# Optimization experiments

Measured on AMD Instinct MI355X. Metric: run time of the kernel, lower is better.

Reference implementation:

```python
import jax, jax.numpy as jnp
import numpy as np

B, C, H, W = 16, 64, 128, 128

def setup_inputs() -> dict:
    key = jax.random.key(0)
    k1, k2, k3 = jax.random.split(key, 3)
    pre = jax.random.normal(k1, (B, C, H, W), dtype=jnp.float32)
    gt = jax.random.normal(k2, (B, C, H, W), dtype=jnp.float32)
    mask = jax.random.randint(k3, (B, C, H, W), 0, 2).astype(jnp.float32)
    return {"pre": pre, "gt": gt, "mask": mask, "batch_size": B}

def reference(pre, gt, mask, batch_size):
    # per-(batch, channel) masked L1 sum, normalized by nonzero count of mask
    # (count clamped to >= 1), summed over all (b, c), divided by batch_size.
    masked_l1 = jnp.sum(jnp.abs(pre - gt) * mask, axis=(2, 3))          # [B, C]
    nonzero = jnp.sum((mask != 0).astype(pre.dtype), axis=(2, 3))       # [B, C]
    denom = jnp.maximum(nonzero, 1.0)
    loss = jnp.sum(masked_l1 / denom) / batch_size
    return loss
```

## Files before the change

### kernel.cpp

```cpp
#include <hip/hip_runtime.h>


#define HW_ELEMS 16384
#define HW_VEC4  4096
#define NBC      1024

__global__ __launch_bounds__(256) void l1_partial_kernel(
    const float* __restrict__ pre,
    const float* __restrict__ gt,
    const float* __restrict__ mask,
    float* __restrict__ ws) {
    const int bc = blockIdx.x;
    const size_t base = (size_t)bc * HW_ELEMS;
    const float4* __restrict__ p4 = (const float4*)(pre + base);
    const float4* __restrict__ g4 = (const float4*)(gt  + base);
    const float4* __restrict__ m4 = (const float4*)(mask + base);

    float s   = 0.0f;
    float cnt = 0.0f;

    for (int i = threadIdx.x; i < HW_VEC4; i += 256) {
        const float4 p = p4[i];
        const float4 g = g4[i];
        const float4 m = m4[i];
        s += fabsf(p.x - g.x) * m.x
           + fabsf(p.y - g.y) * m.y
           + fabsf(p.z - g.z) * m.z
           + fabsf(p.w - g.w) * m.w;
        cnt += (float)(m.x != 0.0f) + (float)(m.y != 0.0f)
             + (float)(m.z != 0.0f) + (float)(m.w != 0.0f);
    }

    #pragma unroll
    for (int off = 32; off > 0; off >>= 1) {
        s   += __shfl_down(s,   off, 64);
        cnt += __shfl_down(cnt, off, 64);
    }

    __shared__ float ss[4];
    __shared__ float sc[4];
    const int wave = threadIdx.x >> 6;
    const int lane = threadIdx.x & 63;
    if (lane == 0) { ss[wave] = s; sc[wave] = cnt; }
    __syncthreads();
    if (threadIdx.x == 0) {
        const float S  = ss[0] + ss[1] + ss[2] + ss[3];
        const float Cn = sc[0] + sc[1] + sc[2] + sc[3];
        ws[bc] = S / fmaxf(Cn, 1.0f);
    }
}

__global__ __launch_bounds__(256) void l1_final_kernel(
    const float* __restrict__ ws,
    const int* __restrict__ bsz,
    float* __restrict__ out) {
    float s = 0.0f;
    for (int i = threadIdx.x; i < NBC; i += 256) s += ws[i];
    #pragma unroll
    for (int off = 32; off > 0; off >>= 1) s += __shfl_down(s, off, 64);
    __shared__ float ss[4];
    const int wave = threadIdx.x >> 6;
    const int lane = threadIdx.x & 63;
    if (lane == 0) ss[wave] = s;
    __syncthreads();
    if (threadIdx.x == 0) {
        out[0] = (ss[0] + ss[1] + ss[2] + ss[3]) / (float)bsz[0];
    }
}

extern "C" void kernel_launch(void* const* d_in, const int* in_sizes, int n_in,
                              void* d_out, int out_size, void* d_ws, size_t ws_size,
                              hipStream_t stream) {
    const float* pre  = (const float*)d_in[0];
    const float* gt   = (const float*)d_in[1];
    const float* mask = (const float*)d_in[2];
    const int*   bsz  = (const int*)d_in[3];
    float* ws  = (float*)d_ws;
    float* out = (float*)d_out;

    l1_partial_kernel<<<NBC, 256, 0, stream>>>(pre, gt, mask, ws);
    l1_final_kernel<<<1, 256, 0, stream>>>(ws, bsz, out);
}
```

Baseline: 200.8 us.

## Split each (b,c) plane across four blocks and batch loads per thread

Each (batch, channel) plane is now handled by four blocks instead of one, giving 4096 blocks to fill the GPU. Each block writes a partial sum and a partial mask count, and the final kernel combines them before normalising. Every thread issues all twelve float4 loads up front to raise memory-level parallelism. The cost is more workspace traffic and a slightly heavier final reduction.

```diff
diff --git a/kernel.cpp b/kernel.cpp
--- a/kernel.cpp
+++ b/kernel.cpp
@@ -1,34 +1,42 @@
 #include <hip/hip_runtime.h>
 
 
-#define HW_ELEMS 16384
-#define HW_VEC4  4096
-#define NBC      1024
+#define NBC        1024
+#define SPLIT      4
+#define NBLK       (NBC * SPLIT)
+#define VEC_PER_BLK 1024
+#define VEC_PER_THR 4
 
 __global__ __launch_bounds__(256) void l1_partial_kernel(
     const float* __restrict__ pre,
     const float* __restrict__ gt,
     const float* __restrict__ mask,
-    float* __restrict__ ws) {
-    const int bc = blockIdx.x;
-    const size_t base = (size_t)bc * HW_ELEMS;
-    const float4* __restrict__ p4 = (const float4*)(pre + base);
-    const float4* __restrict__ g4 = (const float4*)(gt  + base);
-    const float4* __restrict__ m4 = (const float4*)(mask + base);
+    float* __restrict__ s_ws,
+    float* __restrict__ c_ws) {
+    const int blk = blockIdx.x;
+    const size_t v4base = (size_t)blk * VEC_PER_BLK;
+    const float4* __restrict__ p4 = (const float4*)pre  + v4base;
+    const float4* __restrict__ g4 = (const float4*)gt   + v4base;
+    const float4* __restrict__ m4 = (const float4*)mask + v4base;
 
-    float s   = 0.0f;
-    float cnt = 0.0f;
+    float4 P[VEC_PER_THR], G[VEC_PER_THR], M[VEC_PER_THR];
+    #pragma unroll
+    for (int k = 0; k < VEC_PER_THR; ++k) {
+        const int i = threadIdx.x + k * 256;
+        P[k] = p4[i];
+        G[k] = g4[i];
+        M[k] = m4[i];
+    }
 
-    for (int i = threadIdx.x; i < HW_VEC4; i += 256) {
-        const float4 p = p4[i];
-        const float4 g = g4[i];
-        const float4 m = m4[i];
-        s += fabsf(p.x - g.x) * m.x
-           + fabsf(p.y - g.y) * m.y
-           + fabsf(p.z - g.z) * m.z
-           + fabsf(p.w - g.w) * m.w;
-        cnt += (float)(m.x != 0.0f) + (float)(m.y != 0.0f)
-             + (float)(m.z != 0.0f) + (float)(m.w != 0.0f);
+    float s = 0.0f, cnt = 0.0f;
+    #pragma unroll
+    for (int k = 0; k < VEC_PER_THR; ++k) {
+        s += fabsf(P[k].x - G[k].x) * M[k].x
+           + fabsf(P[k].y - G[k].y) * M[k].y
+           + fabsf(P[k].z - G[k].z) * M[k].z
+           + fabsf(P[k].w - G[k].w) * M[k].w;
+        cnt += (float)(M[k].x != 0.0f) + (float)(M[k].y != 0.0f)
+             + (float)(M[k].z != 0.0f) + (float)(M[k].w != 0.0f);
     }
 
     #pragma unroll
@@ -44,24 +52,34 @@
     if (lane == 0) { ss[wave] = s; sc[wave] = cnt; }
     __syncthreads();
     if (threadIdx.x == 0) {
-        const float S  = ss[0] + ss[1] + ss[2] + ss[3];
-        const float Cn = sc[0] + sc[1] + sc[2] + sc[3];
-        ws[bc] = S / fmaxf(Cn, 1.0f);
+        s_ws[blk] = ss[0] + ss[1] + ss[2] + ss[3];
+        c_ws[blk] = sc[0] + sc[1] + sc[2] + sc[3];
     }
 }
 
 __global__ __launch_bounds__(256) void l1_final_kernel(
-    const float* __restrict__ ws,
+    const float* __restrict__ s_ws,
+    const float* __restrict__ c_ws,
     const int* __restrict__ bsz,
     float* __restrict__ out) {
-    float s = 0.0f;
-    for (int i = threadIdx.x; i < NBC; i += 256) s += ws[i];
+    float acc = 0.0f;
     #pragma unroll
-    for (int off = 32; off > 0; off >>= 1) s += __shfl_down(s, off, 64);
+    for (int j = 0; j < NBC / 256; ++j) {
+        const int bc = threadIdx.x + j * 256;
+        float S = 0.0f, Cn = 0.0f;
+        #pragma unroll
+        for (int h = 0; h < SPLIT; ++h) {
+            S  += s_ws[bc * SPLIT + h];
+            Cn += c_ws[bc * SPLIT + h];
+        }
+        acc += S / fmaxf(Cn, 1.0f);
+    }
+    #pragma unroll
+    for (int off = 32; off > 0; off >>= 1) acc += __shfl_down(acc, off, 64);
     __shared__ float ss[4];
     const int wave = threadIdx.x >> 6;
     const int lane = threadIdx.x & 63;
-    if (lane == 0) ss[wave] = s;
+    if (lane == 0) ss[wave] = acc;
     __syncthreads();
     if (threadIdx.x == 0) {
         out[0] = (ss[0] + ss[1] + ss[2] + ss[3]) / (float)bsz[0];
@@ -75,9 +93,10 @@
     const float* gt   = (const float*)d_in[1];
     const float* mask = (const float*)d_in[2];
     const int*   bsz  = (const int*)d_in[3];
-    float* ws  = (float*)d_ws;
-    float* out = (float*)d_out;
+    float* s_ws = (float*)d_ws;
+    float* c_ws = (float*)d_ws + NBLK;
+    float* out  = (float*)d_out;
 
-    l1_partial_kernel<<<NBC, 256, 0, stream>>>(pre, gt, mask, ws);
-    l1_final_kernel<<<1, 256, 0, stream>>>(ws, bsz, out);
+    l1_partial_kernel<<<NBLK, 256, 0, stream>>>(pre, gt, mask, s_ws, c_ws);
+    l1_final_kernel<<<1, 256, 0, stream>>>(s_ws, c_ws, bsz, out);
 }
```

After: 196.0 us. -2.4%, faster.
